# Optimization experiments

Measured on AMD Instinct MI355X. Metric: run time of the kernel, lower is better.

## Reference

```python
import jax, jax.numpy as jnp
import numpy as np

B, V, K, C = 4, 50000, 128, 128
NNZ = 800000
HID = 256
MLP_C = 3 * C  # x_in | x_diffuse | grad_features


def setup_inputs() -> dict:
    key = jax.random.key(0)
    ks = jax.random.split(key, 24)
    inp = {
        "x_in": jax.random.normal(ks[0], (B, V, C), jnp.float32),
        "evals": jax.random.uniform(ks[1], (B, K), jnp.float32) * 10.0,
        "evecs": jax.random.normal(ks[2], (B, V, K), jnp.float32) / np.sqrt(V),
        "mass": jax.random.uniform(ks[3], (B, V), jnp.float32) + 0.1,
    }
    for i, nm in enumerate(["gradX", "gradY", "gradZ"]):
        inp[nm + "_vals"] = jax.random.normal(ks[4 + 3 * i], (B, NNZ), jnp.float32) * 0.1
        inp[nm + "_rows"] = jax.random.randint(ks[5 + 3 * i], (B, NNZ), 0, V, jnp.int32)
        inp[nm + "_cols"] = jax.random.randint(ks[6 + 3 * i], (B, NNZ), 0, V, jnp.int32)
    # learned parameters
    inp["diffusion_time"] = jax.random.uniform(ks[13], (C,), jnp.float32) * 0.1 + 1e-4
    inp["A_weight"] = jax.random.normal(ks[14], (3 * C, 3 * C), jnp.float32) / np.sqrt(3 * C)
    inp["W0"] = jax.random.normal(ks[15], (HID, MLP_C), jnp.float32) / np.sqrt(MLP_C)
    inp["b0"] = jnp.zeros((HID,), jnp.float32)
    inp["W1"] = jax.random.normal(ks[16], (C, HID), jnp.float32) / np.sqrt(HID)
    inp["b1"] = jnp.zeros((C,), jnp.float32)
    return inp


def _spmm(vals, rows, cols, x):
    # per-mesh sparse (V,V) @ dense (V,C) via gather + segment_sum
    def one(v, r, c, xb):
        return jax.ops.segment_sum(v[:, None] * xb[c], r, num_segments=V)
    return jax.vmap(one)(vals, rows, cols, x)


def reference(x_in, evals, evecs, mass,
              gradX_vals, gradX_rows, gradX_cols,
              gradY_vals, gradY_rows, gradY_cols,
              gradZ_vals, gradZ_rows, gradZ_cols,
              diffusion_time, A_weight, W0, b0, W1, b1):
    # --- LearnedTimeDiffusion ---
    t = jnp.maximum(diffusion_time, 1e-8)                      # clamp
    x_spec = jnp.einsum('bvk,bv,bvc->bkc', evecs, mass, x_in)  # to_basis
    coefs = jnp.exp(-evals[:, :, None] * t[None, None, :])     # (B,K,C)
    x_diffuse = jnp.einsum('bvk,bkc->bvc', evecs, coefs * x_spec)  # from_basis
    # --- spatial gradients (sparse ops) ---
    gx = _spmm(gradX_vals, gradX_rows, gradX_cols, x_diffuse)
    gy = _spmm(gradY_vals, gradY_rows, gradY_cols, x_diffuse)
    gz = _spmm(gradZ_vals, gradZ_rows, gradZ_cols, x_diffuse)
    x_grad = jnp.stack((gx, gy, gz), axis=-1)                  # (B,V,C,3)
    # --- SpatialGradientFeatures ---
    vflat = x_grad.reshape(B, V, 3 * C)
    Av = (vflat @ A_weight.T).reshape(B, V, C, 3)
    grad_feats = jnp.tanh(jnp.sum(x_grad * Av, axis=-1))       # (B,V,C)
    # --- MLP + residual (dropout off / eval mode) ---
    f = jnp.concatenate((x_in, x_diffuse, grad_feats), axis=-1)
    h = jax.nn.relu(f @ W0.T + b0)
    out = h @ W1.T + b1
    return out + x_in
```

## Files before the change

kernel.cpp:

```cpp
#include <hip/hip_runtime.h>
#include <cstdint>
#include <cstddef>

#define B_   4
#define V_   50000
#define VP_  50048
#define VPT_ 50176
#define K_   128
#define C_   128
#define NNZ_ 800000
#define HID_ 256

#define NB_   391
#define CAP_  2560
#define CH_   4096
#define NBF_  196

typedef __attribute__((ext_vector_type(8))) short short8;
typedef __attribute__((ext_vector_type(4))) float f32x4;
typedef unsigned short us;

__device__ __forceinline__ us f2b(float f) {
    union { float f; unsigned u; } v; v.f = f;
    unsigned r = v.u + 0x7fffu + ((v.u >> 16) & 1u);
    return (us)(r >> 16);
}
__device__ __forceinline__ float b2f(us h) {
    union { unsigned u; float f; } v; v.u = ((unsigned)h) << 16; return v.f;
}
__device__ __forceinline__ unsigned pk(float lo, float hi) {
    return (unsigned)f2b(lo) | ((unsigned)f2b(hi) << 16);
}
__device__ __forceinline__ short8 cvt8(float4 p0, float4 p1) {
    union { unsigned u[4]; short8 s; } r;
    r.u[0] = pk(p0.x, p0.y); r.u[1] = pk(p0.z, p0.w);
    r.u[2] = pk(p1.x, p1.y); r.u[3] = pk(p1.z, p1.w);
    return r.s;
}

__global__ __launch_bounds__(256) void k_cvt_all(
    const float* __restrict__ W0, const float* __restrict__ W1,
    const float* __restrict__ Aw,
    us* __restrict__ W0b, us* __restrict__ W1b, us* __restrict__ Awb)
{
    int t = blockIdx.x * 256 + threadIdx.x;
    if (t < 16384) {
        const float* src; us* dst; int i8;
        if (t < 12288) { i8 = t * 8;            src = W0 + i8; dst = W0b + i8; }
        else           { i8 = (t - 12288) * 8;  src = W1 + i8; dst = W1b + i8; }
        float4 x0 = *(const float4*)src;
        float4 x1 = *(const float4*)(src + 4);
        uint4 u;
        u.x = pk(x0.x, x0.y); u.y = pk(x0.z, x0.w);
        u.z = pk(x1.x, x1.y); u.w = pk(x1.z, x1.w);
        *(uint4*)dst = u;
    } else {
        int p  = t - 16384;
        int p1 = p / 384, p2 = p - p1 * 384;
        int q1 = 3 * (p1 & 127) + (p1 >> 7);
        int q2 = 3 * (p2 & 127) + (p2 >> 7);
        Awb[p] = f2b(Aw[q1 * 384 + q2]);
    }
}

__global__ __launch_bounds__(256) void k_trans(
    const float* __restrict__ x_in, const float* __restrict__ mass,
    const float* __restrict__ evecs,
    us* __restrict__ mxT, us* __restrict__ evT, us* __restrict__ fb, int b)
{
    const int v0  = blockIdx.x * 64;
    const int tid = threadIdx.x;
    __shared__ us ts[128][72];

#pragma unroll
    for (int it = 0; it < 8; ++it) {
        int f   = tid + it * 256;
        int row = f >> 5;
        int col = (f & 31) * 4;
        int v   = v0 + row;
        float4 x = make_float4(0.f, 0.f, 0.f, 0.f);
        float  m = 0.f;
        if (v < V_) {
            x = *(const float4*)&x_in[((size_t)b * V_ + v) * C_ + col];
            m = mass[b * V_ + v];
            uint2 u; u.x = pk(x.x, x.y); u.y = pk(x.z, x.w);
            *(uint2*)&fb[(size_t)v * 384 + col] = u;
        }
        ts[col + 0][row] = f2b(x.x * m); ts[col + 1][row] = f2b(x.y * m);
        ts[col + 2][row] = f2b(x.z * m); ts[col + 3][row] = f2b(x.w * m);
    }
    __syncthreads();
    {
        int c = tid >> 1, half = tid & 1;
#pragma unroll
        for (int q = 0; q < 4; ++q) {
            uint4 u = *(const uint4*)&ts[c][half * 32 + q * 8];
            *(uint4*)&mxT[(size_t)c * VPT_ + v0 + half * 32 + q * 8] = u;
        }
    }
    __syncthreads();

#pragma unroll
    for (int it = 0; it < 8; ++it) {
        int f   = tid + it * 256;
        int row = f >> 5;
        int col = (f & 31) * 4;
        int v   = v0 + row;
        float4 e = (v < V_)
            ? *(const float4*)&evecs[((size_t)b * V_ + v) * K_ + col]
            : make_float4(0.f, 0.f, 0.f, 0.f);
        ts[col + 0][row] = f2b(e.x); ts[col + 1][row] = f2b(e.y);
        ts[col + 2][row] = f2b(e.z); ts[col + 3][row] = f2b(e.w);
    }
    __syncthreads();
    {
        int k = tid >> 1, half = tid & 1;
#pragma unroll
        for (int q = 0; q < 4; ++q) {
            uint4 u = *(const uint4*)&ts[k][half * 32 + q * 8];
            *(uint4*)&evT[(size_t)k * VPT_ + v0 + half * 32 + q * 8] = u;
        }
    }
}

__global__ __launch_bounds__(256) void k_spec_mfma(
    const us* __restrict__ evT, const us* __restrict__ mxT,
    float* __restrict__ x_spec, int b)
{
    const int vb  = blockIdx.x * 256;
    const int tid = threadIdx.x;
    const int w   = tid >> 6;
    const int lr  = tid & 15;
    const int lk  = (tid & 63) >> 4;

    f32x4 z = {0.f, 0.f, 0.f, 0.f};
    f32x4 acc[2][8];
#pragma unroll
    for (int mi = 0; mi < 2; ++mi)
#pragma unroll
        for (int ni = 0; ni < 8; ++ni) acc[mi][ni] = z;

#pragma unroll 2
    for (int s = 0; s < 8; ++s) {
        int vo = vb + s * 32 + lk * 8;
        short8 a[2], bf[8];
#pragma unroll
        for (int mi = 0; mi < 2; ++mi)
            a[mi] = *(const short8*)&evT[(size_t)(w * 32 + mi * 16 + lr) * VPT_ + vo];
#pragma unroll
        for (int ni = 0; ni < 8; ++ni)
            bf[ni] = *(const short8*)&mxT[(size_t)(ni * 16 + lr) * VPT_ + vo];
#pragma unroll
        for (int mi = 0; mi < 2; ++mi)
#pragma unroll
            for (int ni = 0; ni < 8; ++ni)
                acc[mi][ni] = __builtin_amdgcn_mfma_f32_16x16x32_bf16(
                    a[mi], bf[ni], acc[mi][ni], 0, 0, 0);
    }
#pragma unroll
    for (int mi = 0; mi < 2; ++mi)
#pragma unroll
        for (int ni = 0; ni < 8; ++ni)
#pragma unroll
            for (int r = 0; r < 4; ++r) {
                int k = w * 32 + mi * 16 + lk * 4 + r;
                int c = ni * 16 + lr;
                atomicAdd(&x_spec[((size_t)b * K_ + k) * C_ + c], acc[mi][ni][r]);
            }
}

__global__ __launch_bounds__(256) void k_scale2(
    const float* __restrict__ evals, const float* __restrict__ dt,
    const float* __restrict__ x_spec, us* __restrict__ spec_t, int b)
{
    int i = blockIdx.x * 256 + threadIdx.x;
    int c = i >> 7;
    int k = i & 127;
    float t = fmaxf(dt[c], 1e-8f);
    float v = __expf(-evals[b * K_ + k] * t) * x_spec[((size_t)b * K_ + k) * C_ + c];
    spec_t[i] = f2b(v);
}

__global__ __launch_bounds__(256) void k_frombasis_mfma(
    const float* __restrict__ evecs, const us* __restrict__ spec_t,
    us* __restrict__ fb, int b)
{
    const int v0  = blockIdx.x * 64;
    const int tid = threadIdx.x;
    const int w   = tid >> 6;
    const int lr  = tid & 15;
    const int lk  = (tid & 63) >> 4;

    f32x4 z = {0.f, 0.f, 0.f, 0.f};
    f32x4 acc[4][2];
#pragma unroll
    for (int mi = 0; mi < 4; ++mi)
#pragma unroll
        for (int ni = 0; ni < 2; ++ni) acc[mi][ni] = z;

#pragma unroll
    for (int ks = 0; ks < 4; ++ks) {
        int ko = ks * 32 + lk * 8;
        short8 a[4], bf[2];
#pragma unroll
        for (int mi = 0; mi < 4; ++mi) {
            int v = v0 + mi * 16 + lr;
            float4 p0 = make_float4(0.f, 0.f, 0.f, 0.f);
            float4 p1 = make_float4(0.f, 0.f, 0.f, 0.f);
            if (v < V_) {
                const float* src = &evecs[((size_t)b * V_ + v) * K_ + ko];
                p0 = *(const float4*)src;
                p1 = *(const float4*)(src + 4);
            }
            a[mi] = cvt8(p0, p1);
        }
#pragma unroll
        for (int ni = 0; ni < 2; ++ni)
            bf[ni] = *(const short8*)&spec_t[(size_t)(w * 32 + ni * 16 + lr) * K_ + ko];
#pragma unroll
        for (int mi = 0; mi < 4; ++mi)
#pragma unroll
            for (int ni = 0; ni < 2; ++ni)
                acc[mi][ni] = __builtin_amdgcn_mfma_f32_16x16x32_bf16(
                    a[mi], bf[ni], acc[mi][ni], 0, 0, 0);
    }
#pragma unroll
    for (int mi = 0; mi < 4; ++mi)
#pragma unroll
        for (int ni = 0; ni < 2; ++ni)
#pragma unroll
            for (int r = 0; r < 4; ++r) {
                int v = v0 + mi * 16 + lk * 4 + r;
                int c = w * 32 + ni * 16 + lr;
                if (v < V_) fb[(size_t)v * 384 + 128 + c] = f2b(acc[mi][ni][r]);
            }
}

__global__ __launch_bounds__(256) void k_binfill(
    const int* __restrict__ r0, const int* __restrict__ r1, const int* __restrict__ r2,
    const int* __restrict__ c0, const int* __restrict__ c1, const int* __restrict__ c2,
    const float* __restrict__ v0, const float* __restrict__ v1, const float* __restrict__ v2,
    uint2* __restrict__ chunk, int* __restrict__ gcnt, int b)
{
    const int d   = blockIdx.y;
    const int e0  = blockIdx.x * CH_;
    const int tid = threadIdx.x;
    const int*   rr = (d == 0) ? r0 : (d == 1) ? r1 : r2;
    const int*   cc = (d == 0) ? c0 : (d == 1) ? c1 : c2;
    const float* vv = (d == 0) ? v0 : (d == 1) ? v1 : v2;

    __shared__ int   hist[NB_];
    __shared__ int   cur[NB_];
    __shared__ int   base[NB_];
    __shared__ int   gbase[NB_];
    __shared__ uint2 buf[CH_];

    for (int i = tid; i < NB_; i += 256) { hist[i] = 0; cur[i] = 0; }
    __syncthreads();

    int rloc[16];
#pragma unroll
    for (int j = 0; j < 16; ++j) {
        int e = e0 + j * 256 + tid;
        int r = (e < NNZ_) ? rr[(size_t)b * NNZ_ + e] : -1;
        rloc[j] = r;
        if (r >= 0) atomicAdd(&hist[r >> 7], 1);
    }
    __syncthreads();

    if (tid < 64) {
        int q0 = tid * 7;
        int loc[7];
        int s = 0;
#pragma unroll
        for (int j = 0; j < 7; ++j) {
            int q = q0 + j;
            int h = (q < NB_) ? hist[q] : 0;
            loc[j] = s; s += h;
        }
        int inc = s;
        for (int off = 1; off < 64; off <<= 1) {
            int t = __shfl_up(inc, off, 64);
            if (tid >= off) inc += t;
        }
        int excl = inc - s;
#pragma unroll
        for (int j = 0; j < 7; ++j) {
            int q = q0 + j;
            if (q < NB_) base[q] = excl + loc[j];
        }
    }
    __syncthreads();

#pragma unroll
    for (int j = 0; j < 16; ++j) {
        int r = rloc[j];
        if (r < 0) continue;
        int e = e0 + j * 256 + tid;
        int q = r >> 7;
        int off = atomicAdd(&cur[q], 1);
        int pos = base[q] + off;
        uint2 ent;
        ent.x = __float_as_uint(vv[(size_t)b * NNZ_ + e]);
        ent.y = ((unsigned)q << 23) | ((unsigned)(r & 127) << 16)
              | (unsigned)cc[(size_t)b * NNZ_ + e];
        buf[pos] = ent;
    }
    __syncthreads();

    for (int q = tid; q < NB_; q += 256) {
        int c = cur[q];
        if (c > 0) gbase[q] = atomicAdd(&gcnt[d * NB_ + q], c);
    }
    __syncthreads();

    const int tot = min(CH_, NNZ_ - e0);
#pragma unroll
    for (int j = 0; j < 16; ++j) {
        int i = tid + j * 256;
        if (i >= tot) break;
        uint2 ent = buf[i];
        int q   = ent.y >> 23;
        int dst = gbase[q] + (i - base[q]);
        if (dst < CAP_)
            chunk[(size_t)(d * NB_ + q) * CAP_ + dst] =
                make_uint2(ent.x, ent.y & 0x7fffffu);
    }
}

__global__ __launch_bounds__(256) void k_sortbkt(
    uint2* __restrict__ chunk, const int* __restrict__ gcnt,
    int* __restrict__ ptr)
{
    const int q   = blockIdx.x;
    const int d   = blockIdx.y;
    const int tid = threadIdx.x;
    const int cnt = min(gcnt[d * NB_ + q], CAP_);
    uint2* cb = chunk + (size_t)(d * NB_ + q) * CAP_;
    const int pbase = (d * NB_ + q) * CAP_;

    __shared__ int   hist[129];
    __shared__ int   lcur[128];
    __shared__ uint2 obuf[CAP_];

    for (int i = tid; i < 128; i += 256) { hist[i] = 0; lcur[i] = 0; }
    __syncthreads();

    uint2 ent[10];
    int n = 0;
    for (int i = tid; i < cnt; i += 256) {
        ent[n] = cb[i];
        atomicAdd(&hist[(ent[n].y >> 16) & 127], 1);
        ++n;
    }
    __syncthreads();

    if (tid < 64) {
        int a0 = hist[tid * 2], a1 = hist[tid * 2 + 1];
        int s = a0 + a1;
        int inc = s;
        for (int off = 1; off < 64; off <<= 1) {
            int t = __shfl_up(inc, off, 64);
            if (tid >= off) inc += t;
        }
        int excl = inc - s;
        hist[tid * 2]     = excl;
        hist[tid * 2 + 1] = excl + a0;
        if (tid == 63) hist[128] = inc;
    }
    __syncthreads();

    for (int j = 0; j < n; ++j) {
        int rl  = (ent[j].y >> 16) & 127;
        int dst = hist[rl] + atomicAdd(&lcur[rl], 1);
        obuf[dst] = make_uint2(ent[j].x, ent[j].y & 0xffffu);
    }
    __syncthreads();

    for (int i = tid; i < cnt; i += 256) cb[i] = obuf[i];
    for (int i = tid; i <= 128; i += 256)
        ptr[(d * NB_ + q) * 129 + i] = pbase + hist[i];
}

__global__ __launch_bounds__(256) void k_gather(
    const uint2* __restrict__ chunk, const int* __restrict__ ptr,
    const us* __restrict__ fb, us* __restrict__ vf)
{
    const int d    = blockIdx.y;
    const int w    = threadIdx.x >> 6;
    const int lane = threadIdx.x & 63;
    const int r    = blockIdx.x * 4 + w;
    const int idx  = (d * NB_ + (r >> 7)) * 129 + (r & 127);
    int beg = ptr[idx];
    int end = ptr[idx + 1];
    const int lo2 = lane * 2;

    float ax[8], ay[8];
#pragma unroll
    for (int j = 0; j < 8; ++j) { ax[j] = 0.f; ay[j] = 0.f; }

    int i = beg;
    for (; i + 8 <= end; i += 8) {
        uint2 e[8];
#pragma unroll
        for (int j = 0; j < 8; ++j) e[j] = chunk[i + j];
        unsigned u[8];
#pragma unroll
        for (int j = 0; j < 8; ++j)
            u[j] = *(const unsigned*)&fb[(size_t)e[j].y * 384 + 128 + lo2];
#pragma unroll
        for (int j = 0; j < 8; ++j) {
            float v = __uint_as_float(e[j].x);
            ax[j] += v * b2f((us)(u[j] & 0xffffu));
            ay[j] += v * b2f((us)(u[j] >> 16));
        }
    }
    for (; i < end; ++i) {
        uint2 e0 = chunk[i];
        unsigned u0 = *(const unsigned*)&fb[(size_t)e0.y * 384 + 128 + lo2];
        float v = __uint_as_float(e0.x);
        ax[0] += v * b2f((us)(u0 & 0xffffu));
        ay[0] += v * b2f((us)(u0 >> 16));
    }
    float sx = ((ax[0] + ax[1]) + (ax[2] + ax[3])) + ((ax[4] + ax[5]) + (ax[6] + ax[7]));
    float sy = ((ay[0] + ay[1]) + (ay[2] + ay[3])) + ((ay[4] + ay[5]) + (ay[6] + ay[7]));
    *(unsigned*)&vf[(size_t)r * 384 + d * 128 + lo2] = pk(sx, sy);
}

__global__ __launch_bounds__(256) void k_gf_mfma(
    const us* __restrict__ vf, const us* __restrict__ Awb,
    us* __restrict__ fb)
{
    const int v0  = blockIdx.x * 64;
    const int tid = threadIdx.x;
    const int w   = tid >> 6;
    const int lr  = tid & 15;
    const int lk  = (tid & 63) >> 4;

    f32x4 z = {0.f, 0.f, 0.f, 0.f};
    f32x4 acc[4][3][2];
#pragma unroll
    for (int mi = 0; mi < 4; ++mi)
#pragma unroll
        for (int d = 0; d < 3; ++d)
#pragma unroll
            for (int ci = 0; ci < 2; ++ci) acc[mi][d][ci] = z;

    const us* aa = vf  + (size_t)(v0 + lr) * 384 + lk * 8;
    const us* bb = Awb + (size_t)(w * 32 + lr) * 384 + lk * 8;
#pragma unroll 2
    for (int kc = 0; kc < 12; ++kc) {
        short8 a[4];
#pragma unroll
        for (int mi = 0; mi < 4; ++mi)
            a[mi] = *(const short8*)(aa + mi * (16 * 384) + kc * 32);
        short8 bm[3][2];
#pragma unroll
        for (int d = 0; d < 3; ++d)
#pragma unroll
            for (int ci = 0; ci < 2; ++ci)
                bm[d][ci] = *(const short8*)(bb + (size_t)(d * 128 + ci * 16) * 384 + kc * 32);
#pragma unroll
        for (int mi = 0; mi < 4; ++mi)
#pragma unroll
            for (int d = 0; d < 3; ++d)
#pragma unroll
                for (int ci = 0; ci < 2; ++ci)
                    acc[mi][d][ci] = __builtin_amdgcn_mfma_f32_16x16x32_bf16(
                        a[mi], bm[d][ci], acc[mi][d][ci], 0, 0, 0);
    }
#pragma unroll
    for (int mi = 0; mi < 4; ++mi)
#pragma unroll
        for (int r = 0; r < 4; ++r) {
            int m = mi * 16 + lk * 4 + r;
            int v = v0 + m;
            if (v < V_) {
#pragma unroll
                for (int ci = 0; ci < 2; ++ci) {
                    int c = w * 32 + ci * 16 + lr;
                    float s = 0.f;
#pragma unroll
                    for (int d = 0; d < 3; ++d)
                        s += acc[mi][d][ci][r] * b2f(vf[(size_t)v * 384 + d * 128 + c]);
                    fb[(size_t)v * 384 + 256 + c] = f2b(tanhf(s));
                }
            }
        }
}

__global__ __launch_bounds__(256) void k_mlp_mfma(
    const us* __restrict__ fb,
    const us* __restrict__ W0b, const float* __restrict__ b0,
    const us* __restrict__ W1b, const float* __restrict__ b1,
    const float* __restrict__ x_in, float* __restrict__ out, int b)
{
    const int v0  = blockIdx.x * 64;
    const int tid = threadIdx.x;
    const int w   = tid >> 6;
    const int lr  = tid & 15;
    const int lk  = (tid & 63) >> 4;

    __shared__ us Hs[64][264];

    f32x4 z = {0.f, 0.f, 0.f, 0.f};
    f32x4 acc[4][4];
#pragma unroll
    for (int mi = 0; mi < 4; ++mi)
#pragma unroll
        for (int ni = 0; ni < 4; ++ni) acc[mi][ni] = z;

    const us* fa = fb  + (size_t)(v0 + lr) * 384 + lk * 8;
    const us* wb = W0b + (size_t)(w * 64 + lr) * 384 + lk * 8;
#pragma unroll 4
    for (int kc = 0; kc < 12; ++kc) {
        short8 a[4], bbf[4];
#pragma unroll
        for (int mi = 0; mi < 4; ++mi)
            a[mi] = *(const short8*)(fa + mi * (16 * 384) + kc * 32);
#pragma unroll
        for (int ni = 0; ni < 4; ++ni)
            bbf[ni] = *(const short8*)(wb + ni * (16 * 384) + kc * 32);
#pragma unroll
        for (int mi = 0; mi < 4; ++mi)
#pragma unroll
            for (int ni = 0; ni < 4; ++ni)
                acc[mi][ni] = __builtin_amdgcn_mfma_f32_16x16x32_bf16(
                    a[mi], bbf[ni], acc[mi][ni], 0, 0, 0);
    }
#pragma unroll
    for (int ni = 0; ni < 4; ++ni) {
        int n = w * 64 + ni * 16 + lr;
        float bias = b0[n];
#pragma unroll
        for (int mi = 0; mi < 4; ++mi)
#pragma unroll
            for (int r = 0; r < 4; ++r) {
                int m = mi * 16 + lk * 4 + r;
                Hs[m][n] = f2b(fmaxf(acc[mi][ni][r] + bias, 0.f));
            }
    }
    __syncthreads();

    f32x4 acc2[4][2];
#pragma unroll
    for (int mi = 0; mi < 4; ++mi)
#pragma unroll
        for (int ni = 0; ni < 2; ++ni) acc2[mi][ni] = z;

    const us* w1b = W1b + (size_t)(w * 32 + lr) * 256 + lk * 8;
#pragma unroll 4
    for (int kc = 0; kc < 8; ++kc) {
        short8 a2[4], b2[2];
#pragma unroll
        for (int mi = 0; mi < 4; ++mi)
            a2[mi] = *(const short8*)&Hs[mi * 16 + lr][kc * 32 + lk * 8];
#pragma unroll
        for (int ni = 0; ni < 2; ++ni)
            b2[ni] = *(const short8*)(w1b + ni * (16 * 256) + kc * 32);
#pragma unroll
        for (int mi = 0; mi < 4; ++mi)
#pragma unroll
            for (int ni = 0; ni < 2; ++ni)
                acc2[mi][ni] = __builtin_amdgcn_mfma_f32_16x16x32_bf16(
                    a2[mi], b2[ni], acc2[mi][ni], 0, 0, 0);
    }
#pragma unroll
    for (int ni = 0; ni < 2; ++ni) {
        int n = w * 32 + ni * 16 + lr;
        float bias = b1[n];
#pragma unroll
        for (int mi = 0; mi < 4; ++mi)
#pragma unroll
            for (int r = 0; r < 4; ++r) {
                int m = mi * 16 + lk * 4 + r;
                int v = v0 + m;
                if (v < V_) {
                    size_t o = ((size_t)b * V_ + v) * C_ + n;
                    out[o] = acc2[mi][ni][r] + bias + x_in[o];
                }
            }
    }
}

extern "C" void kernel_launch(void* const* d_in, const int* in_sizes, int n_in,
                              void* d_out, int out_size, void* d_ws, size_t ws_size,
                              hipStream_t stream)
{
    const float* x_in  = (const float*)d_in[0];
    const float* evals = (const float*)d_in[1];
    const float* evecs = (const float*)d_in[2];
    const float* mass  = (const float*)d_in[3];
    const float* gv[3] = {(const float*)d_in[4], (const float*)d_in[7], (const float*)d_in[10]};
    const int*   gr[3] = {(const int*)d_in[5],   (const int*)d_in[8],   (const int*)d_in[11]};
    const int*   gc[3] = {(const int*)d_in[6],   (const int*)d_in[9],   (const int*)d_in[12]};
    const float* dt  = (const float*)d_in[13];
    const float* Aw  = (const float*)d_in[14];
    const float* W0  = (const float*)d_in[15];
    const float* b0  = (const float*)d_in[16];
    const float* W1  = (const float*)d_in[17];
    const float* b1  = (const float*)d_in[18];
    float* out = (float*)d_out;

    float* x_spec = (float*)d_ws;
    us* spec_t = (us*)(x_spec + 65536);
    us* W0b    = spec_t + 16384;
    us* W1b    = W0b + 98304;
    us* Awb    = W1b + 32768;
    us* fb     = Awb + 147456;
    us* vf     = fb + (size_t)VP_ * 384;
    us* evT    = vf + (size_t)VP_ * 384;
    us* mxT    = evT + (size_t)128 * VPT_;
    int* gcnt  = (int*)(mxT + (size_t)128 * VPT_);
    int* ptr   = gcnt + 3 * NB_;
    uint2* chunk = (uint2*)evT;

    hipMemsetAsync(x_spec, 0, 65536 * sizeof(float), stream);
    k_cvt_all<<<dim3(640), 256, 0, stream>>>(W0, W1, Aw, W0b, W1b, Awb);

    for (int b = 0; b < B_; ++b) {
        hipMemsetAsync(gcnt, 0, 3 * NB_ * sizeof(int), stream);
        k_trans<<<dim3(784), 256, 0, stream>>>(x_in, mass, evecs, mxT, evT, fb, b);
        k_spec_mfma<<<dim3(196), 256, 0, stream>>>(evT, mxT, x_spec, b);
        k_scale2<<<dim3(64), 256, 0, stream>>>(evals, dt, x_spec, spec_t, b);
        k_frombasis_mfma<<<dim3(782), 256, 0, stream>>>(evecs, spec_t, fb, b);
        k_binfill<<<dim3(NBF_, 3), 256, 0, stream>>>(
            gr[0], gr[1], gr[2], gc[0], gc[1], gc[2], gv[0], gv[1], gv[2],
            chunk, gcnt, b);
        k_sortbkt<<<dim3(NB_, 3), 256, 0, stream>>>(chunk, gcnt, ptr);
        k_gather<<<dim3(12500, 3), 256, 0, stream>>>(chunk, ptr, fb, vf);
        k_gf_mfma<<<dim3(782), 256, 0, stream>>>(vf, Awb, fb);
        k_mlp_mfma<<<dim3(782), 256, 0, stream>>>(fb, W0b, b0, W1b, b1, x_in, out, b);
    }
}
```

Baseline: 1.507 ms.

## Fuse bucket sort with gather, and gradient features with MLP

The bucket sort kernel now does the sparse gather straight from its shared-memory sorted buffer. This removes the write-back of sorted entries, the row-pointer array and a separate gather launch. The gradient-feature kernel is merged into the MLP kernel, keeping the tanh features in shared memory and feeding them as the last K chunk of the first GEMM instead of writing them to global memory and reading them back. The cost is fewer blocks for the gather (391x3 instead of 12500x3, each looping over 128 rows with 4 waves) and more shared memory per block in the fused MLP kernel, which may lower parallelism and occupancy.

```diff
diff --git a/kernel.cpp b/kernel.cpp
--- a/kernel.cpp
+++ b/kernel.cpp
@@ -328,16 +328,15 @@
     }
 }
 
-__global__ __launch_bounds__(256) void k_sortbkt(
-    uint2* __restrict__ chunk, const int* __restrict__ gcnt,
-    int* __restrict__ ptr)
+__global__ __launch_bounds__(256) void k_sortgather(
+    const uint2* __restrict__ chunk, const int* __restrict__ gcnt,
+    const us* __restrict__ fb, us* __restrict__ vf)
 {
     const int q   = blockIdx.x;
     const int d   = blockIdx.y;
     const int tid = threadIdx.x;
     const int cnt = min(gcnt[d * NB_ + q], CAP_);
-    uint2* cb = chunk + (size_t)(d * NB_ + q) * CAP_;
-    const int pbase = (d * NB_ + q) * CAP_;
+    const uint2* cb = chunk + (size_t)(d * NB_ + q) * CAP_;
 
     __shared__ int   hist[129];
     __shared__ int   lcur[128];
@@ -377,59 +376,53 @@
     }
     __syncthreads();
 
-    for (int i = tid; i < cnt; i += 256) cb[i] = obuf[i];
-    for (int i = tid; i <= 128; i += 256)
-        ptr[(d * NB_ + q) * 129 + i] = pbase + hist[i];
-}
-
-__global__ __launch_bounds__(256) void k_gather(
-    const uint2* __restrict__ chunk, const int* __restrict__ ptr,
-    const us* __restrict__ fb, us* __restrict__ vf)
-{
-    const int d    = blockIdx.y;
-    const int w    = threadIdx.x >> 6;
-    const int lane = threadIdx.x & 63;
-    const int r    = blockIdx.x * 4 + w;
-    const int idx  = (d * NB_ + (r >> 7)) * 129 + (r & 127);
-    int beg = ptr[idx];
-    int end = ptr[idx + 1];
-    const int lo2 = lane * 2;
-
-    float ax[8], ay[8];
-#pragma unroll
-    for (int j = 0; j < 8; ++j) { ax[j] = 0.f; ay[j] = 0.f; }
-
-    int i = beg;
-    for (; i + 8 <= end; i += 8) {
-        uint2 e[8];
-#pragma unroll
-        for (int j = 0; j < 8; ++j) e[j] = chunk[i + j];
-        unsigned u[8];
-#pragma unroll
-        for (int j = 0; j < 8; ++j)
-            u[j] = *(const unsigned*)&fb[(size_t)e[j].y * 384 + 128 + lo2];
-#pragma unroll
-        for (int j = 0; j < 8; ++j) {
-            float v = __uint_as_float(e[j].x);
-            ax[j] += v * b2f((us)(u[j] & 0xffffu));
-            ay[j] += v * b2f((us)(u[j] >> 16));
-        }
-    }
-    for (; i < end; ++i) {
-        uint2 e0 = chunk[i];
-        unsigned u0 = *(const unsigned*)&fb[(size_t)e0.y * 384 + 128 + lo2];
-        float v = __uint_as_float(e0.x);
-        ax[0] += v * b2f((us)(u0 & 0xffffu));
-        ay[0] += v * b2f((us)(u0 >> 16));
-    }
-    float sx = ((ax[0] + ax[1]) + (ax[2] + ax[3])) + ((ax[4] + ax[5]) + (ax[6] + ax[7]));
-    float sy = ((ay[0] + ay[1]) + (ay[2] + ay[3])) + ((ay[4] + ay[5]) + (ay[6] + ay[7]));
-    *(unsigned*)&vf[(size_t)r * 384 + d * 128 + lo2] = pk(sx, sy);
-}
-
-__global__ __launch_bounds__(256) void k_gf_mfma(
+    const int w    = tid >> 6;
+    const int lane = tid & 63;
+    const int lo2  = lane * 2;
+    for (int rl = w; rl < 128; rl += 4) {
+        int r = q * 128 + rl;
+        if (r >= V_) break;
+        int beg = hist[rl], end = hist[rl + 1];
+
+        float ax[8], ay[8];
+#pragma unroll
+        for (int j = 0; j < 8; ++j) { ax[j] = 0.f; ay[j] = 0.f; }
+
+        int i = beg;
+        for (; i + 8 <= end; i += 8) {
+            uint2 e[8];
+#pragma unroll
+            for (int j = 0; j < 8; ++j) e[j] = obuf[i + j];
+            unsigned u[8];
+#pragma unroll
+            for (int j = 0; j < 8; ++j)
+                u[j] = *(const unsigned*)&fb[(size_t)e[j].y * 384 + 128 + lo2];
+#pragma unroll
+            for (int j = 0; j < 8; ++j) {
+                float v = __uint_as_float(e[j].x);
+                ax[j] += v * b2f((us)(u[j] & 0xffffu));
+                ay[j] += v * b2f((us)(u[j] >> 16));
+            }
+        }
+        for (; i < end; ++i) {
+            uint2 e0 = obuf[i];
+            unsigned u0 = *(const unsigned*)&fb[(size_t)e0.y * 384 + 128 + lo2];
+            float v = __uint_as_float(e0.x);
+            ax[0] += v * b2f((us)(u0 & 0xffffu));
+            ay[0] += v * b2f((us)(u0 >> 16));
+        }
+        float sx = ((ax[0] + ax[1]) + (ax[2] + ax[3])) + ((ax[4] + ax[5]) + (ax[6] + ax[7]));
+        float sy = ((ay[0] + ay[1]) + (ay[2] + ay[3])) + ((ay[4] + ay[5]) + (ay[6] + ay[7]));
+        *(unsigned*)&vf[(size_t)r * 384 + d * 128 + lo2] = pk(sx, sy);
+    }
+}
+
+__global__ __launch_bounds__(256) void k_gfmlp(
     const us* __restrict__ vf, const us* __restrict__ Awb,
-    us* __restrict__ fb)
+    const us* __restrict__ fb,
+    const us* __restrict__ W0b, const float* __restrict__ b0,
+    const us* __restrict__ W1b, const float* __restrict__ b1,
+    const float* __restrict__ x_in, float* __restrict__ out, int b)
 {
     const int v0  = blockIdx.x * 64;
     const int tid = threadIdx.x;
@@ -437,87 +430,80 @@
     const int lr  = tid & 15;
     const int lk  = (tid & 63) >> 4;
 
+    __shared__ us gbuf[64][132];
+    __shared__ us Hs[64][264];
+
     f32x4 z = {0.f, 0.f, 0.f, 0.f};
-    f32x4 acc[4][3][2];
-#pragma unroll
-    for (int mi = 0; mi < 4; ++mi)
-#pragma unroll
-        for (int d = 0; d < 3; ++d)
-#pragma unroll
-            for (int ci = 0; ci < 2; ++ci) acc[mi][d][ci] = z;
-
-    const us* aa = vf  + (size_t)(v0 + lr) * 384 + lk * 8;
-    const us* bb = Awb + (size_t)(w * 32 + lr) * 384 + lk * 8;
+
+    {
+        f32x4 acc[4][3][2];
+#pragma unroll
+        for (int mi = 0; mi < 4; ++mi)
+#pragma unroll
+            for (int d2 = 0; d2 < 3; ++d2)
+#pragma unroll
+                for (int ci = 0; ci < 2; ++ci) acc[mi][d2][ci] = z;
+
+        const us* aa = vf  + (size_t)(v0 + lr) * 384 + lk * 8;
+        const us* bb = Awb + (size_t)(w * 32 + lr) * 384 + lk * 8;
 #pragma unroll 2
-    for (int kc = 0; kc < 12; ++kc) {
-        short8 a[4];
-#pragma unroll
-        for (int mi = 0; mi < 4; ++mi)
-            a[mi] = *(const short8*)(aa + mi * (16 * 384) + kc * 32);
-        short8 bm[3][2];
-#pragma unroll
-        for (int d = 0; d < 3; ++d)
-#pragma unroll
-            for (int ci = 0; ci < 2; ++ci)
-                bm[d][ci] = *(const short8*)(bb + (size_t)(d * 128 + ci * 16) * 384 + kc * 32);
-#pragma unroll
-        for (int mi = 0; mi < 4; ++mi)
-#pragma unroll
-            for (int d = 0; d < 3; ++d)
+        for (int kc = 0; kc < 12; ++kc) {
+            short8 a[4];
+#pragma unroll
+            for (int mi = 0; mi < 4; ++mi)
+                a[mi] = *(const short8*)(aa + mi * (16 * 384) + kc * 32);
+            short8 bm[3][2];
+#pragma unroll
+            for (int d2 = 0; d2 < 3; ++d2)
 #pragma unroll
                 for (int ci = 0; ci < 2; ++ci)
-                    acc[mi][d][ci] = __builtin_amdgcn_mfma_f32_16x16x32_bf16(
-                        a[mi], bm[d][ci], acc[mi][d][ci], 0, 0, 0);
-    }
-#pragma unroll
-    for (int mi = 0; mi < 4; ++mi)
-#pragma unroll
-        for (int r = 0; r < 4; ++r) {
-            int m = mi * 16 + lk * 4 + r;
-            int v = v0 + m;
-            if (v < V_) {
+                    bm[d2][ci] = *(const short8*)(bb + (size_t)(d2 * 128 + ci * 16) * 384 + kc * 32);
+#pragma unroll
+            for (int mi = 0; mi < 4; ++mi)
+#pragma unroll
+                for (int d2 = 0; d2 < 3; ++d2)
+#pragma unroll
+                    for (int ci = 0; ci < 2; ++ci)
+                        acc[mi][d2][ci] = __builtin_amdgcn_mfma_f32_16x16x32_bf16(
+                            a[mi], bm[d2][ci], acc[mi][d2][ci], 0, 0, 0);
+        }
+#pragma unroll
+        for (int mi = 0; mi < 4; ++mi)
+#pragma unroll
+            for (int r = 0; r < 4; ++r) {
+                int m = mi * 16 + lk * 4 + r;
+                int v = v0 + m;
 #pragma unroll
                 for (int ci = 0; ci < 2; ++ci) {
                     int c = w * 32 + ci * 16 + lr;
                     float s = 0.f;
 #pragma unroll
-                    for (int d = 0; d < 3; ++d)
-                        s += acc[mi][d][ci][r] * b2f(vf[(size_t)v * 384 + d * 128 + c]);
-                    fb[(size_t)v * 384 + 256 + c] = f2b(tanhf(s));
+                    for (int d2 = 0; d2 < 3; ++d2)
+                        s += acc[mi][d2][ci][r] * b2f(vf[(size_t)v * 384 + d2 * 128 + c]);
+                    gbuf[m][c] = f2b(tanhf(s));
                 }
             }
-        }
-}
-
-__global__ __launch_bounds__(256) void k_mlp_mfma(
-    const us* __restrict__ fb,
-    const us* __restrict__ W0b, const float* __restrict__ b0,
-    const us* __restrict__ W1b, const float* __restrict__ b1,
-    const float* __restrict__ x_in, float* __restrict__ out, int b)
-{
-    const int v0  = blockIdx.x * 64;
-    const int tid = threadIdx.x;
-    const int w   = tid >> 6;
-    const int lr  = tid & 15;
-    const int lk  = (tid & 63) >> 4;
-
-    __shared__ us Hs[64][264];
-
-    f32x4 z = {0.f, 0.f, 0.f, 0.f};
-    f32x4 acc[4][4];
+    }
+    __syncthreads();
+
+    f32x4 acc1[4][4];
 #pragma unroll
     for (int mi = 0; mi < 4; ++mi)
 #pragma unroll
-        for (int ni = 0; ni < 4; ++ni) acc[mi][ni] = z;
+        for (int ni = 0; ni < 4; ++ni) acc1[mi][ni] = z;
 
     const us* fa = fb  + (size_t)(v0 + lr) * 384 + lk * 8;
     const us* wb = W0b + (size_t)(w * 64 + lr) * 384 + lk * 8;
-#pragma unroll 4
+#pragma unroll
     for (int kc = 0; kc < 12; ++kc) {
         short8 a[4], bbf[4];
 #pragma unroll
-        for (int mi = 0; mi < 4; ++mi)
-            a[mi] = *(const short8*)(fa + mi * (16 * 384) + kc * 32);
+        for (int mi = 0; mi < 4; ++mi) {
+            if (kc < 8)
+                a[mi] = *(const short8*)(fa + mi * (16 * 384) + kc * 32);
+            else
+                a[mi] = *(const short8*)&gbuf[mi * 16 + lr][(kc - 8) * 32 + lk * 8];
+        }
 #pragma unroll
         for (int ni = 0; ni < 4; ++ni)
             bbf[ni] = *(const short8*)(wb + ni * (16 * 384) + kc * 32);
@@ -525,8 +511,8 @@
         for (int mi = 0; mi < 4; ++mi)
 #pragma unroll
             for (int ni = 0; ni < 4; ++ni)
-                acc[mi][ni] = __builtin_amdgcn_mfma_f32_16x16x32_bf16(
-                    a[mi], bbf[ni], acc[mi][ni], 0, 0, 0);
+                acc1[mi][ni] = __builtin_amdgcn_mfma_f32_16x16x32_bf16(
+                    a[mi], bbf[ni], acc1[mi][ni], 0, 0, 0);
     }
 #pragma unroll
     for (int ni = 0; ni < 4; ++ni) {
@@ -537,7 +523,7 @@
 #pragma unroll
             for (int r = 0; r < 4; ++r) {
                 int m = mi * 16 + lk * 4 + r;
-                Hs[m][n] = f2b(fmaxf(acc[mi][ni][r] + bias, 0.f));
+                Hs[m][n] = f2b(fmaxf(acc1[mi][ni][r] + bias, 0.f));
             }
     }
     __syncthreads();
@@ -612,7 +598,6 @@
     us* evT    = vf + (size_t)VP_ * 384;
     us* mxT    = evT + (size_t)128 * VPT_;
     int* gcnt  = (int*)(mxT + (size_t)128 * VPT_);
-    int* ptr   = gcnt + 3 * NB_;
     uint2* chunk = (uint2*)evT;
 
     hipMemsetAsync(x_spec, 0, 65536 * sizeof(float), stream);
@@ -627,9 +612,8 @@
         k_binfill<<<dim3(NBF_, 3), 256, 0, stream>>>(
             gr[0], gr[1], gr[2], gc[0], gc[1], gc[2], gv[0], gv[1], gv[2],
             chunk, gcnt, b);
-        k_sortbkt<<<dim3(NB_, 3), 256, 0, stream>>>(chunk, gcnt, ptr);
-        k_gather<<<dim3(12500, 3), 256, 0, stream>>>(chunk, ptr, fb, vf);
-        k_gf_mfma<<<dim3(782), 256, 0, stream>>>(vf, Awb, fb);
-        k_mlp_mfma<<<dim3(782), 256, 0, stream>>>(fb, W0b, b0, W1b, b1, x_in, out, b);
-    }
-}
+        k_sortgather<<<dim3(NB_, 3), 256, 0, stream>>>(chunk, gcnt, fb, vf);
+        k_gfmlp<<<dim3(782), 256, 0, stream>>>(
+            vf, Awb, fb, W0b, b0, W1b, b1, x_in, out, b);
+    }
+}
```

After: 1.533 ms. Within noise of the previous version (+1.7%).
